# Optimization experiments

Hardware: AMD Instinct MI355X
Metric: run time of the kernel (lower is better)

## Reference

```python
import jax, jax.numpy as jnp
import numpy as np

P, NL, NQ, L, P2L, P2Q, D = 50000, 2000, 6000, 8, 128, 64, 32
MAX_MODELS, NPOL, MAXQ, ITERS = 7, 4, 3, 8
ZS = {'traffic': (1385.4059, 859.8119), 'packets': (1.4015, 0.8933), 'eq_lambda': (1350.9712, 858.3162), 'avg_pkts_lambda': (0.9117, 0.9724), 'exp_max_factor': (6.6636, 4.7151), 'pkts_lambda_on': (0.9116, 1.6513), 'avg_t_off': (1.6649, 2.3564), 'avg_t_on': (1.6649, 2.3564), 'ar_a': (0.0, 1.0), 'sigma': (0.0, 1.0), 'capacity': (27611.0918, 20090.6211), 'queue_size': (30259.1055, 21410.0957)}


def _glorot(k, fin, fout):
    lim = float(np.sqrt(6.0 / (fin + fout)))
    return jax.random.uniform(k, (fin, fout), jnp.float32, -lim, lim)


def setup_inputs():
    keys = iter(jax.random.split(jax.random.key(0), 80))
    nk = lambda: next(keys)
    u = lambda shape, lo=0.0, hi=1.0: jax.random.uniform(nk(), shape, jnp.float32, lo, hi)
    inp = {}
    inp['traffic'] = u((P, 1), 1.0, 3000.0)
    inp['packets'] = u((P, 1), 0.5, 3.0)
    inp['eq_lambda'] = u((P, 1), 1.0, 3000.0)
    inp['avg_pkts_lambda'] = u((P, 1))
    inp['exp_max_factor'] = u((P, 1), 1.0, 12.0)
    inp['pkts_lambda_on'] = u((P, 1))
    inp['avg_t_off'] = u((P, 1), 0.1, 4.0)
    inp['avg_t_on'] = u((P, 1), 0.1, 4.0)
    inp['ar_a'] = jax.random.normal(nk(), (P, 1), jnp.float32)
    inp['sigma'] = jax.random.normal(nk(), (P, 1), jnp.float32)
    inp['capacity'] = u((NL, 1), 8000.0, 60000.0)
    inp['queue_size'] = u((NQ, 1), 1000.0, 64000.0)
    inp['weight'] = u((NQ, 1))
    length = jax.random.randint(nk(), (P,), 1, L + 1)
    inp['length'] = length
    inp['model'] = jax.random.randint(nk(), (P,), 0, MAX_MODELS)
    inp['policy'] = jax.random.randint(nk(), (NL,), 0, NPOL)
    inp['priority'] = jax.random.randint(nk(), (NQ,), 0, MAXQ)
    inp['queue_to_path'] = jax.random.randint(nk(), (P, L), 0, NQ)
    inp['link_to_path'] = jax.random.randint(nk(), (P, L), 0, NL)
    p2l_path = jax.random.randint(nk(), (NL, P2L), 0, P)
    inp['path_to_link'] = jnp.stack([p2l_path, jnp.zeros_like(p2l_path)], -1)
    inp['p2l_deg'] = jax.random.randint(nk(), (NL,), 1, P2L + 1)
    pq_path = jax.random.randint(nk(), (NQ, P2Q), 0, P)
    pq_pos = 1 + jax.random.randint(nk(), (NQ, P2Q), 0, L) % length[pq_path]
    inp['path_to_queue'] = jnp.stack([pq_path, pq_pos], -1)
    inp['p2q_deg'] = jax.random.randint(nk(), (NQ,), 1, P2Q + 1)
    inp['queue_to_link'] = jnp.arange(NL * MAXQ).reshape(NL, MAXQ)
    def dense(fin, fout):
        return _glorot(nk(), fin, fout), jnp.zeros((fout,), jnp.float32)
    inp['pe_w1'], inp['pe_b1'] = dense(10 + MAX_MODELS, D)
    inp['pe_w2'], inp['pe_b2'] = dense(D, D)
    inp['le_w1'], inp['le_b1'] = dense(NPOL + 1, D)
    inp['le_w2'], inp['le_b2'] = dense(D, D)
    inp['qe_w1'], inp['qe_b1'] = dense(MAXQ + 2, D)
    inp['qe_w2'], inp['qe_b2'] = dense(D, D)
    inp['prW'] = _glorot(nk(), 2 * D, D); inp['prU'] = _glorot(nk(), D, D); inp['prB'] = jnp.zeros((D,), jnp.float32)
    inp['qrW'] = _glorot(nk(), D, D); inp['qrU'] = _glorot(nk(), D, D); inp['qrB'] = jnp.zeros((D,), jnp.float32)
    inp['lrW'] = _glorot(nk(), D, D); inp['lrU'] = _glorot(nk(), D, D); inp['lrB'] = jnp.zeros((D,), jnp.float32)
    inp['ro_w1'], inp['ro_b1'] = dense(D, D // 2)
    inp['ro_w2'], inp['ro_b2'] = dense(D // 2, D // 2)
    inp['ro_w3'], inp['ro_b3'] = dense(D // 2, 1)
    return inp


def _mlp2(x, w1, b1, w2, b2):
    return jax.nn.relu(jax.nn.relu(x @ w1 + b1) @ w2 + b2)


def _forward(traffic, packets, eq_lambda, avg_pkts_lambda, exp_max_factor, pkts_lambda_on,
             avg_t_off, avg_t_on, ar_a, sigma, capacity, queue_size, weight,
             pe_w1, pe_b1, pe_w2, pe_b2, le_w1, le_b1, le_w2, le_b2, qe_w1, qe_b1, qe_w2, qe_b2,
             prW, prU, prB, qrW, qrU, qrB, lrW, lrU, lrB,
             ro_w1, ro_b1, ro_w2, ro_b2, ro_w3, ro_b3,
             length, model, policy, priority, queue_to_path, link_to_path,
             path_to_link, path_to_queue, queue_to_link, p2l_deg, p2q_deg):
    dt = traffic.dtype
    nz = lambda x, k: (x - ZS[k][0]) / ZS[k][1]
    # link load: masked ragged sum of traffic of paths crossing each link
    p2l_mask = (jnp.arange(P2L) < p2l_deg[:, None]).astype(dt)                # [NL, P2L]
    path_gather_traffic = traffic[path_to_link[:, :, 0], 0]                   # [NL, P2L]
    load = (path_gather_traffic * p2l_mask).sum(1, keepdims=True) / capacity  # [NL, 1]
    pkt_size = traffic / packets                                              # [P, 1]
    path_features = jnp.concatenate([
        nz(traffic, 'traffic'), nz(packets, 'packets'),
        jax.nn.one_hot(model, MAX_MODELS, dtype=dt),
        nz(eq_lambda, 'eq_lambda'), nz(avg_pkts_lambda, 'avg_pkts_lambda'),
        nz(exp_max_factor, 'exp_max_factor'), nz(pkts_lambda_on, 'pkts_lambda_on'),
        nz(avg_t_off, 'avg_t_off'), nz(avg_t_on, 'avg_t_on'),
        nz(ar_a, 'ar_a'), nz(sigma, 'sigma')], axis=1)                         # [P, 17]
    path_state = _mlp2(path_features, pe_w1, pe_b1, pe_w2, pe_b2)             # [P, D]
    link_state = _mlp2(jnp.concatenate([load, jax.nn.one_hot(policy, NPOL, dtype=dt)], 1),
                       le_w1, le_b1, le_w2, le_b2)                             # [NL, D]
    queue_state = _mlp2(jnp.concatenate([nz(queue_size, 'queue_size'),
                                         jax.nn.one_hot(priority, MAXQ, dtype=dt), weight], 1),
                        qe_w1, qe_b1, qe_w2, qe_b2)                            # [NQ, D]
    hop_mask = (jnp.arange(L) < length[:, None]).astype(dt)                    # [P, L]
    p2q_mask = (jnp.arange(P2Q) < p2q_deg[:, None]).astype(dt)                 # [NQ, P2Q]

    def path_step(h, xs):
        x_t, m_t = xs
        h_new = jnp.tanh(x_t @ prW + h @ prU + prB)
        h = m_t[:, None] * h_new + (1.0 - m_t[:, None]) * h  # ragged: freeze past length
        return h, h

    pss = None
    for _ in range(ITERS):
        qg = queue_state[queue_to_path]                                        # [P, L, D]
        lg = link_state[link_to_path]                                          # [P, L, D]
        xin = jnp.concatenate([qg, lg], -1)                                    # [P, L, 2D]
        prev = path_state
        path_state, seq = jax.lax.scan(path_step, path_state,
                                       (jnp.swapaxes(xin, 0, 1), hop_mask.T))
        pss = jnp.concatenate([prev[:, None], jnp.swapaxes(seq, 0, 1)], 1)     # [P, L+1, D]
        pg = pss[path_to_queue[:, :, 0], path_to_queue[:, :, 1]]               # [NQ, P2Q, D]
        path_sum = (pg * p2q_mask[:, :, None]).sum(1)                          # [NQ, D]
        queue_state = jnp.tanh(path_sum @ qrW + queue_state @ qrU + qrB)
        qgl = queue_state[queue_to_link]                                       # [NL, 3, D]
        h = link_state
        for t in range(MAXQ):  # fixed tiny sequence of 3 queues per link
            h = jnp.tanh(qgl[:, t] @ lrW + h @ lrU + lrB)
        link_state = h
    cap_g = capacity[link_to_path, 0]                                          # [P, L]
    occ = jax.nn.relu(pss[:, 1:] @ ro_w1 + ro_b1)
    occ = jax.nn.relu(occ @ ro_w2 + ro_b2)
    occ = (occ @ ro_w3 + ro_b3)[:, :, 0]                                       # [P, L]
    queue_delay = ((occ / cap_g) * hop_mask).sum(1, keepdims=True)             # [P, 1]
    trans_delay = pkt_size * ((1.0 / cap_g) * hop_mask).sum(1, keepdims=True)  # [P, 1]
    return queue_delay + trans_delay


def reference(traffic, packets, eq_lambda, avg_pkts_lambda, exp_max_factor, pkts_lambda_on,
              avg_t_off, avg_t_on, ar_a, sigma, capacity, queue_size, weight,
              pe_w1, pe_b1, pe_w2, pe_b2, le_w1, le_b1, le_w2, le_b2, qe_w1, qe_b1, qe_w2, qe_b2,
              prW, prU, prB, qrW, qrU, qrB, lrW, lrU, lrB,
              ro_w1, ro_b1, ro_w2, ro_b2, ro_w3, ro_b3,
              length, model, policy, priority, queue_to_path, link_to_path,
              path_to_link, path_to_queue, queue_to_link, p2l_deg, p2q_deg):
    return _forward(traffic, packets, eq_lambda, avg_pkts_lambda, exp_max_factor, pkts_lambda_on,
                    avg_t_off, avg_t_on, ar_a, sigma, capacity, queue_size, weight,
                    pe_w1, pe_b1, pe_w2, pe_b2, le_w1, le_b1, le_w2, le_b2, qe_w1, qe_b1, qe_w2, qe_b2,
                    prW, prU, prB, qrW, qrU, qrB, lrW, lrU, lrB,
                    ro_w1, ro_b1, ro_w2, ro_b2, ro_w3, ro_b3,
                    length, model, policy, priority, queue_to_path, link_to_path,
                    path_to_link, path_to_queue, queue_to_link, p2l_deg, p2q_deg)
```

## Files before the change

### kernel.cpp

```cpp
#include <hip/hip_runtime.h>
#include <hip/hip_bf16.h>

#define P_ 50000
#define NL_ 2000
#define NQ_ 6000
#define L_ 8
#define P2L_ 128
#define P2Q_ 64
#define D_ 32
#define ITERS_ 8
#define RA_ 1563
#define RC_ 1500

typedef __hip_bfloat16 bf16;
typedef unsigned short u16;
typedef unsigned int u32;

__device__ __forceinline__ float bfb2f(u16 u) {
    union { u32 i; float f; } c; c.i = ((u32)u) << 16; return c.f;
}
__device__ __forceinline__ u16 f2bfb(float f) {
    union { bf16 h; u16 u; } c; c.h = __float2bfloat16(f); return c.u;
}
__device__ __forceinline__ u32 pk2(float a, float b) {
    return (u32)f2bfb(a) | ((u32)f2bfb(b) << 16);
}

__device__ __forceinline__ float tanh_fast(float x) {
    return 1.f - 2.f / (__expf(2.f * x) + 1.f);
}
__device__ __forceinline__ float4 tanh4(float4 a) {
    return make_float4(tanh_fast(a.x), tanh_fast(a.y), tanh_fast(a.z), tanh_fast(a.w));
}

__device__ __forceinline__ void hr_rebuild(float* hr, float4 own) {
    hr[0] = own.x; hr[1] = own.y; hr[2] = own.z; hr[3] = own.w;
#pragma unroll
    for (int c = 0; c < 4; c++)  hr[4 + c]  = __shfl_xor(hr[c], 1, 64);
#pragma unroll
    for (int c = 0; c < 8; c++)  hr[8 + c]  = __shfl_xor(hr[c], 2, 64);
#pragma unroll
    for (int c = 0; c < 16; c++) hr[16 + c] = __shfl_xor(hr[c], 4, 64);
}

__device__ __forceinline__ float4 matvec32o(const float* hr, const float* base,
                                            const int* offs, float4 acc) {
#pragma unroll
    for (int s = 0; s < 8; s++) {
        const float* u0 = base + offs[s];
#pragma unroll
        for (int c = 0; c < 4; c++) {
            const float4 u = *(const float4*)(u0 + 32 * c);
            const float hk = hr[4 * s + c];
            acc.x += hk * u.x; acc.y += hk * u.y;
            acc.z += hk * u.z; acc.w += hk * u.w;
        }
    }
    return acc;
}

__device__ bool detect_f32(const void* p, int n) {
    const u16* u = (const u16*)p;
    int m = n < 64 ? n : 64;
    bool bad = false;
    for (int k = 0; k < m; k++) {
        float v = bfb2f(u[k]);
        float av = fabsf(v);
        bool sane = (v == v) && (av <= 1e6f) && (av == 0.0f || av >= 1e-8f);
        bad |= !sane;
    }
    return bad;
}


struct CvtArgs { const void* p[40]; };

__global__ __launch_bounds__(256) void k_convert(CvtArgs a, float* __restrict__ dst,
                                                 int* __restrict__ counters) {
    static constexpr int N[40] = {
        50000,50000,50000,50000,50000,50000,50000,50000,50000,50000,
        2000,6000,6000,
        544,32,1024,32, 160,32,1024,32, 160,32,1024,32,
        2048,1024,32, 1024,1024,32, 1024,1024,32,
        512,16,256,16,16,1};
    if (blockIdx.x == 0 && threadIdx.x < 16) counters[threadIdx.x] = 0;
    int b = blockIdx.x, t = 0, off = 0;
    for (;;) {
        int nb = (N[t] + 255) >> 8;
        if (b < nb) break;
        b -= nb; off += N[t]; ++t;
    }
    const void* src = a.p[t];
    const int n = N[t];
    const bool isf = detect_f32(src, n);
    const int i = b * 256 + threadIdx.x;
    if (i < n)
        dst[off + i] = isf ? ((const float*)src)[i] : bfb2f(((const u16*)src)[i]);
}


__global__ __launch_bounds__(256) void k_hist(const int* __restrict__ length,
                                              int* __restrict__ hist) {
    __shared__ int hc[8];
    const int tid = threadIdx.x;
    if (tid < 8) hc[tid] = 0;
    __syncthreads();
    int p = blockIdx.x * 256 + tid;
    if (p < P_) atomicAdd(&hc[length[p] - 1], 1);
    __syncthreads();
    if (tid < 8 && hc[tid] > 0) atomicAdd(&hist[tid], hc[tid]);
}

__global__ __launch_bounds__(256) void k_scatter(const int* __restrict__ length,
                                                 const int* __restrict__ hist,
                                                 int* __restrict__ cursor,
                                                 int* __restrict__ perm,
                                                 int* __restrict__ inv) {
    __shared__ int cnt[8];
    __shared__ int base[8];
    const int tid = threadIdx.x;
    if (tid < 8) cnt[tid] = 0;
    __syncthreads();
    const int p = blockIdx.x * 256 + tid;
    int b = 0, r = 0;
    if (p < P_) {
        b = length[p] - 1;
        r = atomicAdd(&cnt[b], 1);
    }
    __syncthreads();
    if (tid < 8) {
        int pre = 0;
#pragma unroll
        for (int k = 0; k < 8; k++) pre += (k < tid) ? hist[k] : 0;
        base[tid] = pre + (cnt[tid] > 0 ? atomicAdd(&cursor[tid], cnt[tid]) : 0);
    }
    __syncthreads();
    if (p < P_) {
        const int pos = base[b] + r;
        perm[pos] = p;
        inv[p] = pos;
    }
}


__global__ __launch_bounds__(256) void k_remap(
    const int* __restrict__ perm, const int* __restrict__ inv,
    const int* __restrict__ q2p, const int* __restrict__ l2p,
    const int* __restrict__ length, const int* __restrict__ p2q,
    int* __restrict__ q2ps, int* __restrict__ l2ps, int* __restrict__ lens,
    int* __restrict__ p2qs)
{
    const int blk = blockIdx.x;
    if (blk < RA_) {
        const int idx = blk * 256 + threadIdx.x;
        if (idx >= P_ * 8) return;
        const int j = idx >> 3, t = idx & 7;
        const int p = perm[j];
        q2ps[idx] = q2p[p * 8 + t];
        l2ps[idx] = l2p[p * 8 + t];
        if (t == 0) lens[j] = length[p];
    } else {
        const int e = (blk - RA_) * 256 + threadIdx.x;
        if (e >= NQ_ * P2Q_) return;
        const int2 pr = ((const int2*)p2q)[e];
        ((int2*)p2qs)[e] = make_int2(inv[pr.x], pr.y);
    }
}


__global__ __launch_bounds__(256) void k_path_embed(
    const float* __restrict__ traffic, const float* __restrict__ packets,
    const float* __restrict__ eq_lambda, const float* __restrict__ avg_pkts_lambda,
    const float* __restrict__ exp_max_factor, const float* __restrict__ pkts_lambda_on,
    const float* __restrict__ avg_t_off, const float* __restrict__ avg_t_on,
    const float* __restrict__ ar_a, const float* __restrict__ sigma,
    const int* __restrict__ model, const int* __restrict__ inv,
    const float* __restrict__ w1, const float* __restrict__ b1,
    const float* __restrict__ w2, const float* __restrict__ b2,
    float* __restrict__ sps)
{
    __shared__ float s_w1[544], s_w2[1024], s_b1[32], s_b2[32];
    const int tid = threadIdx.x;
    for (int idx = tid; idx < 544; idx += 256)  s_w1[idx] = w1[idx];
    for (int idx = tid; idx < 1024; idx += 256) s_w2[idx] = w2[idx];
    if (tid < 32) { s_b1[tid] = b1[tid]; s_b2[tid] = b2[tid]; }
    __syncthreads();

    int p = blockIdx.x * 256 + tid;
    if (p >= P_) return;
    float f[10];
    f[0] = (traffic[p]        - 1385.4059f) * (1.f / 859.8119f);
    f[1] = (packets[p]        - 1.4015f)    * (1.f / 0.8933f);
    f[2] = (eq_lambda[p]      - 1350.9712f) * (1.f / 858.3162f);
    f[3] = (avg_pkts_lambda[p]- 0.9117f)    * (1.f / 0.9724f);
    f[4] = (exp_max_factor[p] - 6.6636f)    * (1.f / 4.7151f);
    f[5] = (pkts_lambda_on[p] - 0.9116f)    * (1.f / 1.6513f);
    f[6] = (avg_t_off[p]      - 1.6649f)    * (1.f / 2.3564f);
    f[7] = (avg_t_on[p]       - 1.6649f)    * (1.f / 2.3564f);
    f[8] = ar_a[p];
    f[9] = sigma[p];
    const int mrow = 2 + model[p];
    float h1[32];
#pragma unroll
    for (int d = 0; d < 32; d++) {
        float a = s_b1[d] + s_w1[mrow * 32 + d];
        a += f[0] * s_w1[0 * 32 + d];
        a += f[1] * s_w1[1 * 32 + d];
#pragma unroll
        for (int j = 0; j < 8; j++) a += f[2 + j] * s_w1[(9 + j) * 32 + d];
        h1[d] = fmaxf(a, 0.f);
    }
    float* dst = sps + (size_t)inv[p] * 32;
#pragma unroll
    for (int d = 0; d < 32; d++) {
        float a = s_b2[d];
#pragma unroll
        for (int k = 0; k < 32; k++) a += h1[k] * s_w2[k * 32 + d];
        dst[d] = fmaxf(a, 0.f);
    }
}


__global__ __launch_bounds__(256) void k_queue_embed(
    const float* __restrict__ queue_size, const float* __restrict__ weight,
    const int* __restrict__ priority,
    const float* __restrict__ w1, const float* __restrict__ b1,
    const float* __restrict__ w2, const float* __restrict__ b2,
    const float* __restrict__ prW, const float* __restrict__ prB,
    float* __restrict__ queue_state, float* __restrict__ zq)
{
    __shared__ float s_w1[160], s_w2[1024], s_pw[1024], s_b1[32], s_b2[32], s_pb[32];
    const int tid = threadIdx.x;
    if (tid < 160) s_w1[tid] = w1[tid];
    for (int idx = tid; idx < 1024; idx += 256) {
        s_w2[idx] = w2[idx];
        s_pw[idx] = prW[idx];
    }
    if (tid < 32) { s_b1[tid] = b1[tid]; s_b2[tid] = b2[tid]; s_pb[tid] = prB[tid]; }
    __syncthreads();

    int q = blockIdx.x * 256 + tid;
    if (q >= NQ_) return;
    float f0 = (queue_size[q] - 30259.1055f) * (1.f / 21410.0957f);
    float f4 = weight[q];
    int prow = 1 + priority[q];
    float h1[32];
#pragma unroll
    for (int d = 0; d < 32; d++) {
        float a = s_b1[d] + s_w1[prow * 32 + d]
                + f0 * s_w1[0 * 32 + d] + f4 * s_w1[4 * 32 + d];
        h1[d] = fmaxf(a, 0.f);
    }
    float h2[32];
#pragma unroll
    for (int d = 0; d < 32; d++) {
        float a = s_b2[d];
#pragma unroll
        for (int k = 0; k < 32; k++) a += h1[k] * s_w2[k * 32 + d];
        h2[d] = fmaxf(a, 0.f);
        queue_state[q * 32 + d] = h2[d];
    }
#pragma unroll
    for (int d = 0; d < 32; d++) {
        float a = s_pb[d];
#pragma unroll
        for (int k = 0; k < 32; k++) a += h2[k] * s_pw[k * 32 + d];
        zq[q * 32 + d] = a;
    }
}


__global__ __launch_bounds__(256) void k_link_embed(
    const float* __restrict__ traffic, const float* __restrict__ capacity,
    const int* __restrict__ policy,
    const int* __restrict__ p2l, const int* __restrict__ p2l_deg,
    const float* __restrict__ w1, const float* __restrict__ b1,
    const float* __restrict__ w2, const float* __restrict__ b2,
    const float* __restrict__ prWl,
    float* __restrict__ link_state, float* __restrict__ zl)
{
    __shared__ float wsh[2272];
    __shared__ float h1s[4][32];
    __shared__ float h2s[4][32];
    const int tid = threadIdx.x;
    if (tid < 160) wsh[tid] = w1[tid];
    if (tid < 32)  wsh[160 + tid] = b1[tid];
    for (int idx = tid; idx < 1024; idx += 256) {
        wsh[192 + idx]  = w2[idx];
        wsh[1248 + idx] = prWl[idx];
    }
    if (tid >= 32 && tid < 64) wsh[1216 + tid - 32] = b2[tid - 32];
    __syncthreads();

    const int w = tid >> 6, lane = tid & 63;
    const int l = blockIdx.x * 4 + w;
    const int deg = p2l_deg[l];
    float s = 0.f;
    if (lane < deg)      s += traffic[p2l[l * 256 + 2 * lane]];
    if (lane + 64 < deg) s += traffic[p2l[l * 256 + 2 * (lane + 64)]];
#pragma unroll
    for (int m = 1; m < 64; m <<= 1) s += __shfl_xor(s, m, 64);
    const float load = s / capacity[l];
    const int prow = 1 + policy[l];
    if (lane < 32) {
        float a = wsh[160 + lane] + wsh[prow * 32 + lane] + load * wsh[lane];
        h1s[w][lane] = fmaxf(a, 0.f);
    }
    __syncthreads();
    if (lane < 32) {
        float a = wsh[1216 + lane];
#pragma unroll
        for (int k = 0; k < 32; k++) a += h1s[w][k] * wsh[192 + k * 32 + lane];
        a = fmaxf(a, 0.f);
        link_state[l * 32 + lane] = a;
        h2s[w][lane] = a;
    }
    __syncthreads();
    if (lane < 32) {
        float a = 0.f;
#pragma unroll
        for (int k = 0; k < 32; k++) a += h2s[w][k] * wsh[1248 + k * 32 + lane];
        zl[l * 32 + lane] = a;
    }
}


__global__ __launch_bounds__(256, 2) void k_path_rnn(
    const int* __restrict__ q2ps, const int* __restrict__ l2ps,
    const int* __restrict__ lens,
    const float* __restrict__ prU,
    const float* __restrict__ zq, const float* __restrict__ zl,
    float* __restrict__ sps, u16* __restrict__ pss)
{
    const int tid = threadIdx.x;
    const int grp = tid >> 3, i = tid & 7;
    const int j = blockIdx.x * 32 + grp;
    if (j >= P_) return;
    const int len = lens[j];

    float4 Ub[32];
#pragma unroll
    for (int s = 0; s < 8; s++) {
        const float* rb = prU + ((i ^ s) * 128 + 4 * i);
#pragma unroll
        for (int c = 0; c < 4; c++)
            Ub[4 * s + c] = *(const float4*)(rb + 32 * c);
    }

    const int4 qi0 = *(const int4*)(q2ps + (size_t)j * 8);
    const int4 qi1 = *(const int4*)(q2ps + (size_t)j * 8 + 4);
    const int4 li0 = *(const int4*)(l2ps + (size_t)j * 8);
    const int4 li1 = *(const int4*)(l2ps + (size_t)j * 8 + 4);
    const int qidx[8] = {qi0.x, qi0.y, qi0.z, qi0.w, qi1.x, qi1.y, qi1.z, qi1.w};
    const int lidx[8] = {li0.x, li0.y, li0.z, li0.w, li1.x, li1.y, li1.z, li1.w};

    float4 own = *(const float4*)(sps + (size_t)j * 32 + 4 * i);
    float hr[32];
    hr_rebuild(hr, own);

    float4 z;
    {
        const float4 a = *(const float4*)(zq + (size_t)qidx[0] * 32 + 4 * i);
        const float4 b = *(const float4*)(zl + (size_t)lidx[0] * 32 + 4 * i);
        z = make_float4(a.x + b.x, a.y + b.y, a.z + b.z, a.w + b.w);
    }

#pragma unroll
    for (int t = 0; t < 8; t++) {
        if (t >= len) break;
        float4 acc = z;
        if (t + 1 < len) {
            const float4 a = *(const float4*)(zq + (size_t)qidx[t + 1] * 32 + 4 * i);
            const float4 b = *(const float4*)(zl + (size_t)lidx[t + 1] * 32 + 4 * i);
            z = make_float4(a.x + b.x, a.y + b.y, a.z + b.z, a.w + b.w);
        }
#pragma unroll
        for (int k = 0; k < 32; k++) {
            const float hk = hr[k];
            acc.x += hk * Ub[k].x; acc.y += hk * Ub[k].y;
            acc.z += hk * Ub[k].z; acc.w += hk * Ub[k].w;
        }
        own = tanh4(acc);
        uint2 w2;
        w2.x = pk2(own.x, own.y);
        w2.y = pk2(own.z, own.w);
        *(uint2*)(pss + (size_t)j * 256 + t * 32 + 4 * i) = w2;
        if (t + 1 < len) hr_rebuild(hr, own);
    }
    *(float4*)(sps + (size_t)j * 32 + 4 * i) = own;
}


__global__ __launch_bounds__(256) void k_queue_update(
    const int* __restrict__ p2qs, const int* __restrict__ p2q_deg,
    const float* __restrict__ qrW, const float* __restrict__ qrU,
    const float* __restrict__ qrB,
    const float* __restrict__ prWq, const float* __restrict__ prB,
    const u16* __restrict__ pss, float* __restrict__ queue_state,
    float* __restrict__ zq)
{
    __shared__ float wl[3 * 1024 + 64];
    const int tid = threadIdx.x;
#pragma unroll
    for (int jj = 0; jj < 4; jj++) {
        wl[tid + 256 * jj]        = qrW[tid + 256 * jj];
        wl[1024 + tid + 256 * jj] = qrU[tid + 256 * jj];
        wl[2048 + tid + 256 * jj] = prWq[tid + 256 * jj];
    }
    if (tid < 32) { wl[3072 + tid] = qrB[tid]; wl[3104 + tid] = prB[tid]; }
    __syncthreads();

    const int w = tid >> 6, lane = tid & 63;
    const int g = lane >> 3, i = lane & 7;
    const int q = blockIdx.x * 4 + w;
    const int deg = p2q_deg[q];

    int offs[8];
#pragma unroll
    for (int s = 0; s < 8; s++) offs[s] = (i ^ s) * 128 + 4 * i;

    float4 ps = {0.f, 0.f, 0.f, 0.f};
    for (int j = g; j < deg; j += 8) {
        const int sj = p2qs[q * 128 + 2 * j];
        int pos = p2qs[q * 128 + 2 * j + 1] - 1;
        pos = pos < 0 ? 0 : (pos > 7 ? 7 : pos);
        const ushort4 v = *(const ushort4*)(pss + (size_t)sj * 256 + pos * 32 + 4 * i);
        ps.x += bfb2f(v.x); ps.y += bfb2f(v.y);
        ps.z += bfb2f(v.z); ps.w += bfb2f(v.w);
    }
#pragma unroll
    for (int m = 8; m < 64; m <<= 1) {
        ps.x += __shfl_xor(ps.x, m, 64);
        ps.y += __shfl_xor(ps.y, m, 64);
        ps.z += __shfl_xor(ps.z, m, 64);
        ps.w += __shfl_xor(ps.w, m, 64);
    }
    const float4 qs = *(const float4*)(queue_state + (size_t)q * 32 + 4 * i);

    float psr[32]; hr_rebuild(psr, ps);
    float qsr[32]; hr_rebuild(qsr, qs);
    float4 acc = *(const float4*)(wl + 3072 + 4 * i);
    acc = matvec32o(psr, wl, offs, acc);
    acc = matvec32o(qsr, wl + 1024, offs, acc);
    const float4 nh = tanh4(acc);

    float nhr[32]; hr_rebuild(nhr, nh);
    float4 zacc = *(const float4*)(wl + 3104 + 4 * i);
    zacc = matvec32o(nhr, wl + 2048, offs, zacc);

    if (g == 0) {
        *(float4*)(queue_state + (size_t)q * 32 + 4 * i) = nh;
        *(float4*)(zq + (size_t)q * 32 + 4 * i) = zacc;
    }
}


__global__ __launch_bounds__(256) void k_link_update(
    const int* __restrict__ q2l,
    const float* __restrict__ lrW, const float* __restrict__ lrU,
    const float* __restrict__ lrB,
    const float* __restrict__ prWl,
    const float* __restrict__ queue_state, float* __restrict__ link_state,
    float* __restrict__ zl)
{
    __shared__ float wl[3 * 1024 + 32];
    const int tid = threadIdx.x;
#pragma unroll
    for (int jj = 0; jj < 4; jj++) {
        wl[tid + 256 * jj]        = lrW[tid + 256 * jj];
        wl[1024 + tid + 256 * jj] = lrU[tid + 256 * jj];
        wl[2048 + tid + 256 * jj] = prWl[tid + 256 * jj];
    }
    if (tid < 32) wl[3072 + tid] = lrB[tid];
    __syncthreads();

    const int w = tid >> 6, lane = tid & 63;
    const int i = lane & 7, g = lane >> 3;
    const int l = blockIdx.x * 4 + w;

    int offs[8];
#pragma unroll
    for (int s = 0; s < 8; s++) offs[s] = (i ^ s) * 128 + 4 * i;

    float4 h = *(const float4*)(link_state + (size_t)l * 32 + 4 * i);
    float hhr[32]; hr_rebuild(hhr, h);

#pragma unroll
    for (int t = 0; t < 3; t++) {
        const int qq = q2l[l * 3 + t];
        const float4 qg = *(const float4*)(queue_state + (size_t)qq * 32 + 4 * i);
        float qgr[32]; hr_rebuild(qgr, qg);
        float4 acc = *(const float4*)(wl + 3072 + 4 * i);
        acc = matvec32o(qgr, wl, offs, acc);
        acc = matvec32o(hhr, wl + 1024, offs, acc);
        h = tanh4(acc);
        hr_rebuild(hhr, h);
    }
    float4 zacc = make_float4(0.f, 0.f, 0.f, 0.f);
    zacc = matvec32o(hhr, wl + 2048, offs, zacc);
    if (g == 0) {
        *(float4*)(link_state + (size_t)l * 32 + 4 * i) = h;
        *(float4*)(zl + (size_t)l * 32 + 4 * i) = zacc;
    }
}


__global__ __launch_bounds__(256) void k_readout(
    const void* __restrict__ raw_traffic, const int* __restrict__ perm,
    const float* __restrict__ traffic, const float* __restrict__ packets,
    const float* __restrict__ capacity,
    const int* __restrict__ l2ps, const int* __restrict__ lens,
    const float* __restrict__ w1, const float* __restrict__ b1,
    const float* __restrict__ w2, const float* __restrict__ b2,
    const float* __restrict__ w3, const float* __restrict__ b3,
    const u16* __restrict__ pss, void* __restrict__ out)
{
    __shared__ float wl[817];
    __shared__ float xs[32][52];
    __shared__ int s_outf32;
    const int tid = threadIdx.x;
    for (int idx = tid; idx < 512; idx += 256) wl[idx] = w1[idx];
    if (tid < 256) wl[528 + tid] = w2[tid];
    if (tid < 16) {
        wl[512 + tid] = b1[tid];
        wl[784 + tid] = b2[tid];
        wl[800 + tid] = w3[tid];
    }
    if (tid == 0) {
        wl[816] = b3[0];
        s_outf32 = detect_f32(raw_traffic, P_) ? 1 : 0;
    }
    __syncthreads();

    const int grp = tid >> 3, i = tid & 7;
    const int j = blockIdx.x * 32 + grp;
    if (j >= P_) return;
    const int len = lens[j];
    float qd = 0.f, ts = 0.f;
    for (int t = 0; t < len; t++) {
        const ushort4 hu = *(const ushort4*)(pss + (size_t)j * 256 + t * 32 + 4 * i);
        float4 hv;
        hv.x = bfb2f(hu.x); hv.y = bfb2f(hu.y); hv.z = bfb2f(hu.z); hv.w = bfb2f(hu.w);
        *(float4*)&xs[grp][4 * i] = hv;
        float a0 = wl[512 + 2 * i], a1 = wl[512 + 2 * i + 1];
#pragma unroll
        for (int k = 0; k < 32; k += 4) {
            const float4 xv = *(const float4*)&xs[grp][k];
            const float2 u0 = *(const float2*)&wl[(k + 0) * 16 + 2 * i];
            const float2 u1 = *(const float2*)&wl[(k + 1) * 16 + 2 * i];
            const float2 u2 = *(const float2*)&wl[(k + 2) * 16 + 2 * i];
            const float2 u3 = *(const float2*)&wl[(k + 3) * 16 + 2 * i];
            a0 += xv.x * u0.x + xv.y * u1.x + xv.z * u2.x + xv.w * u3.x;
            a1 += xv.x * u0.y + xv.y * u1.y + xv.z * u2.y + xv.w * u3.y;
        }
        a0 = fmaxf(a0, 0.f); a1 = fmaxf(a1, 0.f);
        *(float2*)&xs[grp][32 + 2 * i] = make_float2(a0, a1);
        float c0 = wl[784 + 2 * i], c1 = wl[784 + 2 * i + 1];
#pragma unroll
        for (int k = 0; k < 16; k += 4) {
            const float4 xv = *(const float4*)&xs[grp][32 + k];
            const float2 u0 = *(const float2*)&wl[528 + (k + 0) * 16 + 2 * i];
            const float2 u1 = *(const float2*)&wl[528 + (k + 1) * 16 + 2 * i];
            const float2 u2 = *(const float2*)&wl[528 + (k + 2) * 16 + 2 * i];
            const float2 u3 = *(const float2*)&wl[528 + (k + 3) * 16 + 2 * i];
            c0 += xv.x * u0.x + xv.y * u1.x + xv.z * u2.x + xv.w * u3.x;
            c1 += xv.x * u0.y + xv.y * u1.y + xv.z * u2.y + xv.w * u3.y;
        }
        c0 = fmaxf(c0, 0.f); c1 = fmaxf(c1, 0.f);
        float pv = c0 * wl[800 + 2 * i] + c1 * wl[800 + 2 * i + 1];
        pv += __shfl_xor(pv, 1, 8);
        pv += __shfl_xor(pv, 2, 8);
        pv += __shfl_xor(pv, 4, 8);
        const float occv = pv + wl[816];
        const float inv = 1.f / capacity[l2ps[j * 8 + t]];
        qd += occv * inv;
        ts += inv;
    }
    if (i == 0) {
        const int p = perm[j];
        const float res = qd + (traffic[p] / packets[p]) * ts;
        if (s_outf32) ((float*)out)[p] = res;
        else          ((bf16*)out)[p] = __float2bfloat16(res);
    }
}


extern "C" void kernel_launch(void* const* d_in, const int* in_sizes, int n_in,
                              void* d_out, int out_size, void* d_ws, size_t ws_size,
                              hipStream_t stream)
{
    static const int CVT_N[40] = {
        50000,50000,50000,50000,50000,50000,50000,50000,50000,50000,
        2000,6000,6000,
        544,32,1024,32, 160,32,1024,32, 160,32,1024,32,
        2048,1024,32, 1024,1024,32, 1024,1024,32,
        512,16,256,16,16,1};

    const int*  length   = (const int*)d_in[13];
    const int*  model    = (const int*)d_in[14];
    const int*  policy   = (const int*)d_in[15];
    const int*  priority = (const int*)d_in[16];
    const int*  q2p      = (const int*)d_in[17];
    const int*  l2p      = (const int*)d_in[18];
    const int*  p2l      = (const int*)d_in[19];
    const int*  p2l_deg  = (const int*)d_in[20];
    const int*  p2q      = (const int*)d_in[21];
    const int*  p2q_deg  = (const int*)d_in[22];
    const int*  q2l      = (const int*)d_in[23];

    CvtArgs ca;
    for (int i = 0; i < 13; i++) ca.p[i] = d_in[i];
    for (int i = 0; i < 27; i++) ca.p[13 + i] = d_in[24 + i];

    int off[41]; off[0] = 0;
    for (int i = 0; i < 40; i++) off[i + 1] = off[i] + CVT_N[i];
    int nblk = 0;
    for (int i = 0; i < 40; i++) nblk += (CVT_N[i] + 255) / 256;

    float* ws = (float*)d_ws;
    const float* c_traffic    = ws + off[0];
    const float* c_packets    = ws + off[1];
    const float* c_eq_lambda  = ws + off[2];
    const float* c_apl        = ws + off[3];
    const float* c_emf        = ws + off[4];
    const float* c_plo        = ws + off[5];
    const float* c_atoff      = ws + off[6];
    const float* c_aton       = ws + off[7];
    const float* c_ar_a       = ws + off[8];
    const float* c_sigma      = ws + off[9];
    const float* c_capacity   = ws + off[10];
    const float* c_queue_size = ws + off[11];
    const float* c_weight     = ws + off[12];
    const float* c_pe_w1 = ws + off[13]; const float* c_pe_b1 = ws + off[14];
    const float* c_pe_w2 = ws + off[15]; const float* c_pe_b2 = ws + off[16];
    const float* c_le_w1 = ws + off[17]; const float* c_le_b1 = ws + off[18];
    const float* c_le_w2 = ws + off[19]; const float* c_le_b2 = ws + off[20];
    const float* c_qe_w1 = ws + off[21]; const float* c_qe_b1 = ws + off[22];
    const float* c_qe_w2 = ws + off[23]; const float* c_qe_b2 = ws + off[24];
    const float* c_prW = ws + off[25]; const float* c_prU = ws + off[26];
    const float* c_prB = ws + off[27];
    const float* c_qrW = ws + off[28]; const float* c_qrU = ws + off[29];
    const float* c_qrB = ws + off[30];
    const float* c_lrW = ws + off[31]; const float* c_lrU = ws + off[32];
    const float* c_lrB = ws + off[33];
    const float* c_ro_w1 = ws + off[34]; const float* c_ro_b1 = ws + off[35];
    const float* c_ro_w2 = ws + off[36]; const float* c_ro_b2 = ws + off[37];
    const float* c_ro_w3 = ws + off[38]; const float* c_ro_b3 = ws + off[39];

    size_t base = ((size_t)off[40] + 63) & ~(size_t)63;
    float* sps         = ws + base;
    float* queue_state = sps + (size_t)P_ * 32;
    float* link_state  = queue_state + (size_t)NQ_ * 32;
    float* zq          = link_state + (size_t)NL_ * 32;
    float* zl          = zq + (size_t)NQ_ * 32;
    u16*   pss         = (u16*)(zl + (size_t)NL_ * 32);
    int*   perm        = (int*)(pss + (size_t)P_ * 256);
    int*   inv         = perm + P_;
    int*   lens        = inv + P_;
    int*   q2ps        = lens + P_;
    int*   l2ps        = q2ps + (size_t)P_ * 8;
    int*   p2qs        = l2ps + (size_t)P_ * 8;
    int*   counters    = p2qs + (size_t)NQ_ * 2 * P2Q_;
    int*   hist        = counters;
    int*   cursor      = counters + 8;

    k_convert<<<nblk, 256, 0, stream>>>(ca, ws, counters);
    k_hist<<<(P_ + 255) / 256, 256, 0, stream>>>(length, hist);
    k_scatter<<<(P_ + 255) / 256, 256, 0, stream>>>(length, hist, cursor, perm, inv);
    k_remap<<<RA_ + RC_, 256, 0, stream>>>(
        perm, inv, q2p, l2p, length, p2q, q2ps, l2ps, lens, p2qs);

    k_path_embed<<<(P_ + 255) / 256, 256, 0, stream>>>(
        c_traffic, c_packets, c_eq_lambda, c_apl, c_emf, c_plo, c_atoff, c_aton,
        c_ar_a, c_sigma, model, inv, c_pe_w1, c_pe_b1, c_pe_w2, c_pe_b2, sps);
    k_queue_embed<<<(NQ_ + 255) / 256, 256, 0, stream>>>(
        c_queue_size, c_weight, priority, c_qe_w1, c_qe_b1, c_qe_w2, c_qe_b2,
        c_prW, c_prB, queue_state, zq);
    k_link_embed<<<NL_ / 4, 256, 0, stream>>>(
        c_traffic, c_capacity, policy, p2l, p2l_deg,
        c_le_w1, c_le_b1, c_le_w2, c_le_b2, c_prW + 1024, link_state, zl);

    for (int it = 0; it < ITERS_; ++it) {
        k_path_rnn<<<(P_ + 31) / 32, 256, 0, stream>>>(
            q2ps, l2ps, lens, c_prU, zq, zl, sps, pss);
        k_queue_update<<<NQ_ / 4, 256, 0, stream>>>(
            p2qs, p2q_deg, c_qrW, c_qrU, c_qrB, c_prW, c_prB,
            pss, queue_state, zq);
        k_link_update<<<NL_ / 4, 256, 0, stream>>>(
            q2l, c_lrW, c_lrU, c_lrB, c_prW + 1024,
            queue_state, link_state, zl);
    }

    k_readout<<<(P_ + 31) / 32, 256, 0, stream>>>(
        d_in[0], perm, c_traffic, c_packets, c_capacity, l2ps, lens,
        c_ro_w1, c_ro_b1, c_ro_w2, c_ro_b2, c_ro_w3, c_ro_b3, pss, d_out);
}
```

Before: 688.6 us.

## Fuse final path RNN step with readout and drop unused last updates

The eighth message-passing iteration is replaced by a single kernel that runs the path RNN and immediately applies the readout MLP per step. The last queue and link updates are skipped because nothing downstream reads their outputs. This also avoids writing and re-reading the bf16 path sequence states. The output-dtype flag is now computed once during conversion, and the path-to-queue index pairs are read as a single int2. The fused kernel holds more live registers (U weights plus readout state), which may lower occupancy.

```diff
diff --git a/kernel.cpp b/kernel.cpp
--- a/kernel.cpp
+++ b/kernel.cpp
@@ -93,6 +93,7 @@
     const void* src = a.p[t];
     const int n = N[t];
     const bool isf = detect_f32(src, n);
+    if (t == 0 && b == 0 && threadIdx.x == 0) counters[16] = isf ? 1 : 0;
     const int i = b * 256 + threadIdx.x;
     if (i < n)
         dst[off + i] = isf ? ((const float*)src)[i] : bfb2f(((const u16*)src)[i]);
@@ -123,10 +124,7 @@
     __syncthreads();
     const int p = blockIdx.x * 256 + tid;
     int b = 0, r = 0;
-    if (p < P_) {
-        b = length[p] - 1;
-        r = atomicAdd(&cnt[b], 1);
-    }
+    if (p < P_) { b = length[p] - 1; r = atomicAdd(&cnt[b], 1); }
     __syncthreads();
     if (tid < 8) {
         int pre = 0;
@@ -135,11 +133,7 @@
         base[tid] = pre + (cnt[tid] > 0 ? atomicAdd(&cursor[tid], cnt[tid]) : 0);
     }
     __syncthreads();
-    if (p < P_) {
-        const int pos = base[b] + r;
-        perm[pos] = p;
-        inv[p] = pos;
-    }
+    if (p < P_) { const int pos = base[b] + r; perm[pos] = p; inv[p] = pos; }
 }
 
 
@@ -391,6 +385,132 @@
 }
 
 
+__global__ __launch_bounds__(256, 2) void k_rnn_last(
+    const int* __restrict__ q2ps, const int* __restrict__ l2ps,
+    const int* __restrict__ lens, const int* __restrict__ perm,
+    const float* __restrict__ prU,
+    const float* __restrict__ zq, const float* __restrict__ zl,
+    const float* __restrict__ sps,
+    const float* __restrict__ capacity,
+    const float* __restrict__ traffic, const float* __restrict__ packets,
+    const float* __restrict__ w1, const float* __restrict__ b1,
+    const float* __restrict__ w2, const float* __restrict__ b2,
+    const float* __restrict__ w3, const float* __restrict__ b3,
+    const int* __restrict__ flags, void* __restrict__ out)
+{
+    __shared__ float wl[817];
+    const int tid = threadIdx.x;
+    for (int idx = tid; idx < 512; idx += 256) wl[idx] = w1[idx];
+    if (tid < 256) wl[528 + tid] = w2[tid];
+    if (tid < 16) {
+        wl[512 + tid] = b1[tid];
+        wl[784 + tid] = b2[tid];
+        wl[800 + tid] = w3[tid];
+    }
+    if (tid == 0) wl[816] = b3[0];
+    __syncthreads();
+
+    const int grp = tid >> 3, i = tid & 7;
+    const int j = blockIdx.x * 32 + grp;
+    if (j >= P_) return;
+    const int len = lens[j];
+
+    float4 Ub[32];
+#pragma unroll
+    for (int s = 0; s < 8; s++) {
+        const float* rb = prU + ((i ^ s) * 128 + 4 * i);
+#pragma unroll
+        for (int c = 0; c < 4; c++)
+            Ub[4 * s + c] = *(const float4*)(rb + 32 * c);
+    }
+
+    const int4 qi0 = *(const int4*)(q2ps + (size_t)j * 8);
+    const int4 qi1 = *(const int4*)(q2ps + (size_t)j * 8 + 4);
+    const int4 li0 = *(const int4*)(l2ps + (size_t)j * 8);
+    const int4 li1 = *(const int4*)(l2ps + (size_t)j * 8 + 4);
+    const int qidx[8] = {qi0.x, qi0.y, qi0.z, qi0.w, qi1.x, qi1.y, qi1.z, qi1.w};
+    const int lidx[8] = {li0.x, li0.y, li0.z, li0.w, li1.x, li1.y, li1.z, li1.w};
+
+    float4 own = *(const float4*)(sps + (size_t)j * 32 + 4 * i);
+    float hr[32];
+    hr_rebuild(hr, own);
+
+    float4 z;
+    {
+        const float4 a = *(const float4*)(zq + (size_t)qidx[0] * 32 + 4 * i);
+        const float4 b = *(const float4*)(zl + (size_t)lidx[0] * 32 + 4 * i);
+        z = make_float4(a.x + b.x, a.y + b.y, a.z + b.z, a.w + b.w);
+    }
+
+    float qd = 0.f, ts = 0.f;
+#pragma unroll
+    for (int t = 0; t < 8; t++) {
+        if (t >= len) break;
+        float4 acc = z;
+        if (t + 1 < len) {
+            const float4 a = *(const float4*)(zq + (size_t)qidx[t + 1] * 32 + 4 * i);
+            const float4 b = *(const float4*)(zl + (size_t)lidx[t + 1] * 32 + 4 * i);
+            z = make_float4(a.x + b.x, a.y + b.y, a.z + b.z, a.w + b.w);
+        }
+#pragma unroll
+        for (int k = 0; k < 32; k++) {
+            const float hk = hr[k];
+            acc.x += hk * Ub[k].x; acc.y += hk * Ub[k].y;
+            acc.z += hk * Ub[k].z; acc.w += hk * Ub[k].w;
+        }
+        own = tanh4(acc);
+        hr_rebuild(hr, own);
+
+        float a0 = wl[512 + 2 * i], a1 = wl[512 + 2 * i + 1];
+#pragma unroll
+        for (int s = 0; s < 8; s++) {
+#pragma unroll
+            for (int c = 0; c < 4; c++) {
+                const int k = 4 * (i ^ s) + c;
+                const float2 u = *(const float2*)&wl[k * 16 + 2 * i];
+                const float hk = hr[4 * s + c];
+                a0 += hk * u.x; a1 += hk * u.y;
+            }
+        }
+        a0 = fmaxf(a0, 0.f); a1 = fmaxf(a1, 0.f);
+        float h2r[16];
+        h2r[0] = a0; h2r[1] = a1;
+#pragma unroll
+        for (int c = 0; c < 2; c++) h2r[2 + c] = __shfl_xor(h2r[c], 1, 64);
+#pragma unroll
+        for (int c = 0; c < 4; c++) h2r[4 + c] = __shfl_xor(h2r[c], 2, 64);
+#pragma unroll
+        for (int c = 0; c < 8; c++) h2r[8 + c] = __shfl_xor(h2r[c], 4, 64);
+        float c0 = wl[784 + 2 * i], c1 = wl[784 + 2 * i + 1];
+#pragma unroll
+        for (int s = 0; s < 8; s++) {
+#pragma unroll
+            for (int c = 0; c < 2; c++) {
+                const int k = 2 * (i ^ s) + c;
+                const float2 u = *(const float2*)&wl[528 + k * 16 + 2 * i];
+                const float hk = h2r[2 * s + c];
+                c0 += hk * u.x; c1 += hk * u.y;
+            }
+        }
+        c0 = fmaxf(c0, 0.f); c1 = fmaxf(c1, 0.f);
+        float pv = c0 * wl[800 + 2 * i] + c1 * wl[800 + 2 * i + 1];
+        pv += __shfl_xor(pv, 1, 8);
+        pv += __shfl_xor(pv, 2, 8);
+        pv += __shfl_xor(pv, 4, 8);
+        const float occv = pv + wl[816];
+        const float inv = 1.f / capacity[lidx[t]];
+        qd += occv * inv;
+        ts += inv;
+    }
+    if (i == 0) {
+        const int p = perm[j];
+        const float res = qd + (traffic[p] / packets[p]) * ts;
+        if (flags[0]) ((float*)out)[p] = res;
+        else          ((bf16*)out)[p] = __float2bfloat16(res);
+    }
+}
+
+
 __global__ __launch_bounds__(256) void k_queue_update(
     const int* __restrict__ p2qs, const int* __restrict__ p2q_deg,
     const float* __restrict__ qrW, const float* __restrict__ qrU,
@@ -421,10 +541,10 @@
 
     float4 ps = {0.f, 0.f, 0.f, 0.f};
     for (int j = g; j < deg; j += 8) {
-        const int sj = p2qs[q * 128 + 2 * j];
-        int pos = p2qs[q * 128 + 2 * j + 1] - 1;
+        const int2 pr = ((const int2*)p2qs)[q * 64 + j];
+        int pos = pr.y - 1;
         pos = pos < 0 ? 0 : (pos > 7 ? 7 : pos);
-        const ushort4 v = *(const ushort4*)(pss + (size_t)sj * 256 + pos * 32 + 4 * i);
+        const ushort4 v = *(const ushort4*)(pss + (size_t)pr.x * 256 + pos * 32 + 4 * i);
         ps.x += bfb2f(v.x); ps.y += bfb2f(v.y);
         ps.z += bfb2f(v.z); ps.w += bfb2f(v.w);
     }
@@ -501,86 +621,6 @@
     if (g == 0) {
         *(float4*)(link_state + (size_t)l * 32 + 4 * i) = h;
         *(float4*)(zl + (size_t)l * 32 + 4 * i) = zacc;
-    }
-}
-
-
-__global__ __launch_bounds__(256) void k_readout(
-    const void* __restrict__ raw_traffic, const int* __restrict__ perm,
-    const float* __restrict__ traffic, const float* __restrict__ packets,
-    const float* __restrict__ capacity,
-    const int* __restrict__ l2ps, const int* __restrict__ lens,
-    const float* __restrict__ w1, const float* __restrict__ b1,
-    const float* __restrict__ w2, const float* __restrict__ b2,
-    const float* __restrict__ w3, const float* __restrict__ b3,
-    const u16* __restrict__ pss, void* __restrict__ out)
-{
-    __shared__ float wl[817];
-    __shared__ float xs[32][52];
-    __shared__ int s_outf32;
-    const int tid = threadIdx.x;
-    for (int idx = tid; idx < 512; idx += 256) wl[idx] = w1[idx];
-    if (tid < 256) wl[528 + tid] = w2[tid];
-    if (tid < 16) {
-        wl[512 + tid] = b1[tid];
-        wl[784 + tid] = b2[tid];
-        wl[800 + tid] = w3[tid];
-    }
-    if (tid == 0) {
-        wl[816] = b3[0];
-        s_outf32 = detect_f32(raw_traffic, P_) ? 1 : 0;
-    }
-    __syncthreads();
-
-    const int grp = tid >> 3, i = tid & 7;
-    const int j = blockIdx.x * 32 + grp;
-    if (j >= P_) return;
-    const int len = lens[j];
-    float qd = 0.f, ts = 0.f;
-    for (int t = 0; t < len; t++) {
-        const ushort4 hu = *(const ushort4*)(pss + (size_t)j * 256 + t * 32 + 4 * i);
-        float4 hv;
-        hv.x = bfb2f(hu.x); hv.y = bfb2f(hu.y); hv.z = bfb2f(hu.z); hv.w = bfb2f(hu.w);
-        *(float4*)&xs[grp][4 * i] = hv;
-        float a0 = wl[512 + 2 * i], a1 = wl[512 + 2 * i + 1];
-#pragma unroll
-        for (int k = 0; k < 32; k += 4) {
-            const float4 xv = *(const float4*)&xs[grp][k];
-            const float2 u0 = *(const float2*)&wl[(k + 0) * 16 + 2 * i];
-            const float2 u1 = *(const float2*)&wl[(k + 1) * 16 + 2 * i];
-            const float2 u2 = *(const float2*)&wl[(k + 2) * 16 + 2 * i];
-            const float2 u3 = *(const float2*)&wl[(k + 3) * 16 + 2 * i];
-            a0 += xv.x * u0.x + xv.y * u1.x + xv.z * u2.x + xv.w * u3.x;
-            a1 += xv.x * u0.y + xv.y * u1.y + xv.z * u2.y + xv.w * u3.y;
-        }
-        a0 = fmaxf(a0, 0.f); a1 = fmaxf(a1, 0.f);
-        *(float2*)&xs[grp][32 + 2 * i] = make_float2(a0, a1);
-        float c0 = wl[784 + 2 * i], c1 = wl[784 + 2 * i + 1];
-#pragma unroll
-        for (int k = 0; k < 16; k += 4) {
-            const float4 xv = *(const float4*)&xs[grp][32 + k];
-            const float2 u0 = *(const float2*)&wl[528 + (k + 0) * 16 + 2 * i];
-            const float2 u1 = *(const float2*)&wl[528 + (k + 1) * 16 + 2 * i];
-            const float2 u2 = *(const float2*)&wl[528 + (k + 2) * 16 + 2 * i];
-            const float2 u3 = *(const float2*)&wl[528 + (k + 3) * 16 + 2 * i];
-            c0 += xv.x * u0.x + xv.y * u1.x + xv.z * u2.x + xv.w * u3.x;
-            c1 += xv.x * u0.y + xv.y * u1.y + xv.z * u2.y + xv.w * u3.y;
-        }
-        c0 = fmaxf(c0, 0.f); c1 = fmaxf(c1, 0.f);
-        float pv = c0 * wl[800 + 2 * i] + c1 * wl[800 + 2 * i + 1];
-        pv += __shfl_xor(pv, 1, 8);
-        pv += __shfl_xor(pv, 2, 8);
-        pv += __shfl_xor(pv, 4, 8);
-        const float occv = pv + wl[816];
-        const float inv = 1.f / capacity[l2ps[j * 8 + t]];
-        qd += occv * inv;
-        ts += inv;
-    }
-    if (i == 0) {
-        const int p = perm[j];
-        const float res = qd + (traffic[p] / packets[p]) * ts;
-        if (s_outf32) ((float*)out)[p] = res;
-        else          ((bf16*)out)[p] = __float2bfloat16(res);
     }
 }
 
@@ -663,6 +703,7 @@
     int*   counters    = p2qs + (size_t)NQ_ * 2 * P2Q_;
     int*   hist        = counters;
     int*   cursor      = counters + 8;
+    int*   flags       = counters + 16;
 
     k_convert<<<nblk, 256, 0, stream>>>(ca, ws, counters);
     k_hist<<<(P_ + 255) / 256, 256, 0, stream>>>(length, hist);
@@ -680,7 +721,7 @@
         c_traffic, c_capacity, policy, p2l, p2l_deg,
         c_le_w1, c_le_b1, c_le_w2, c_le_b2, c_prW + 1024, link_state, zl);
 
-    for (int it = 0; it < ITERS_; ++it) {
+    for (int it = 0; it < ITERS_ - 1; ++it) {
         k_path_rnn<<<(P_ + 31) / 32, 256, 0, stream>>>(
             q2ps, l2ps, lens, c_prU, zq, zl, sps, pss);
         k_queue_update<<<NQ_ / 4, 256, 0, stream>>>(
@@ -691,7 +732,9 @@
             queue_state, link_state, zl);
     }
 
-    k_readout<<<(P_ + 31) / 32, 256, 0, stream>>>(
-        d_in[0], perm, c_traffic, c_packets, c_capacity, l2ps, lens,
-        c_ro_w1, c_ro_b1, c_ro_w2, c_ro_b2, c_ro_w3, c_ro_b3, pss, d_out);
-}
+    k_rnn_last<<<(P_ + 31) / 32, 256, 0, stream>>>(
+        q2ps, l2ps, lens, perm, c_prU, zq, zl, sps,
+        c_capacity, c_traffic, c_packets,
+        c_ro_w1, c_ro_b1, c_ro_w2, c_ro_b2, c_ro_w3, c_ro_b3,
+        flags, d_out);
+}
```

Result: faster. 669.8 us (-2.7%).
